# Kernel optimization log

Hardware: AMD Instinct MI355X
Metric: run time of the kernel (lower is better)

## Reference

```python
import jax, jax.numpy as jnp
import numpy as np

B, C, L = 4, 256, 2048
HEADS, DIM_HEAD = 8, 64
HIDDEN = HEADS * DIM_HEAD  # 512


def setup_inputs() -> dict:
    key = jax.random.key(0)
    k1, k2, k3, k4 = jax.random.split(key, 4)
    x = jax.random.normal(k1, (B, C, L), dtype=jnp.float32)
    # Conv1d kernel_size=1 weights, squeezed to [out_ch, in_ch]
    w_qkv = jax.random.normal(k2, (3 * HIDDEN, C), dtype=jnp.float32) * (1.0 / np.sqrt(C))
    w_out = jax.random.normal(k3, (C, HIDDEN), dtype=jnp.float32) * (1.0 / np.sqrt(HIDDEN))
    b_out = jax.random.normal(k4, (C,), dtype=jnp.float32) * 0.01
    return {"x": x, "w_qkv": w_qkv, "w_out": w_out, "b_out": b_out}


def reference(x, w_qkv, w_out, b_out):
    b, c, l = x.shape
    scale = DIM_HEAD ** (-0.5)
    # pointwise conv == channel matmul
    qkv = jnp.einsum('oc,bcl->bol', w_qkv, x)  # [b, 3*hidden, l]
    q, k, v = jnp.split(qkv, 3, axis=1)        # each [b, hidden, l]
    def to_heads(t):
        return t.reshape(b, HEADS, DIM_HEAD, l)  # b h d l
    q, k, v = to_heads(q), to_heads(k), to_heads(v)
    q = q * scale
    sim = jnp.einsum('bhdi,bhdj->bhij', q, k)   # [b,h,l,l]
    attn = jax.nn.softmax(sim, axis=-1)          # stable softmax (max-subtract inside)
    out = jnp.einsum('bhij,bhdj->bhid', attn, v)  # [b,h,l,d]
    out = out.transpose(0, 1, 3, 2).reshape(b, HIDDEN, l)  # b (h d) l
    return jnp.einsum('oc,bcl->bol', w_out, out) + b_out[None, :, None]
```

## Files before the change

### kernel.cpp

```cpp
#include <hip/hip_runtime.h>

typedef unsigned short u16;
typedef unsigned int u32;
typedef __bf16 bf16x8 __attribute__((ext_vector_type(8)));
typedef float f32x4 __attribute__((ext_vector_type(4)));
typedef float f32x16 __attribute__((ext_vector_type(16)));

#define MFMA16(a, b, c) __builtin_amdgcn_mfma_f32_16x16x32_bf16((a), (b), (c), 0, 0, 0)
#define MFMA32(a, b, c) __builtin_amdgcn_mfma_f32_32x32x16_bf16((a), (b), (c), 0, 0, 0)

#define Bn 4
#define Cn 256
#define Ln 2048
#define Hn 8
#define Dn 64
#define HID 512
#define SEGELEMS 4194304

__device__ __forceinline__ u16 bf16_rne(float f) {
  u32 u = __builtin_bit_cast(u32, f);
  u += 0x7FFFu + ((u >> 16) & 1u);
  return (u16)(u >> 16);
}

__device__ __forceinline__ unsigned pack2(float a, float b) {
  return (unsigned)bf16_rne(a) | ((unsigned)bf16_rne(b) << 16);
}

__device__ __forceinline__ u32 pkperm(float lo, float hi) {
  u32 a = __builtin_bit_cast(u32, lo) + 0x8000u;
  u32 b = __builtin_bit_cast(u32, hi) + 0x8000u;
#if __has_builtin(__builtin_amdgcn_perm)
  return __builtin_amdgcn_perm(b, a, 0x07060302u);
#else
  return (b & 0xFFFF0000u) | (a >> 16);
#endif
}

__device__ __forceinline__ float bf16_up(u16 v) {
  u32 u = ((u32)v) << 16;
  return __builtin_bit_cast(float, u);
}

__device__ __forceinline__ float fast_exp2(float x) {
#if __has_builtin(__builtin_amdgcn_exp2f)
  return __builtin_amdgcn_exp2f(x);
#else
  return exp2f(x);
#endif
}

__device__ __forceinline__ float fast_rcp(float x) {
#if __has_builtin(__builtin_amdgcn_rcpf)
  return __builtin_amdgcn_rcpf(x);
#else
  return 1.0f / x;
#endif
}

__device__ __forceinline__ void async_load16(const u16* g, u16* l) {
  __builtin_amdgcn_global_load_lds(
      (const __attribute__((address_space(1))) void*)g,
      (__attribute__((address_space(3))) void*)l, 16, 0, 0);
}

__global__ __launch_bounds__(256) void prep_all(const float* __restrict__ wqkv,
                                                const float* __restrict__ wout,
                                                const float* __restrict__ x,
                                                u16* __restrict__ wq,
                                                u16* __restrict__ wo,
                                                u16* __restrict__ xT) {
  const int t = threadIdx.x;
  if (blockIdx.x < 2048) {
    int i = blockIdx.x * 256 + t;
    const float QSCALE = 0.125f * 1.44269504088896340736f;
    if (i < 3 * HID * Cn) {
      float v = wqkv[i];
      if (i < HID * Cn) v *= QSCALE;
      wq[i] = bf16_rne(v);
    } else {
      int j = i - 3 * HID * Cn;
      wo[j] = bf16_rne(wout[j]);
    }
    return;
  }
  __shared__ u16 tile[64][72];
  int v = blockIdx.x - 2048;
  const int lt = v & 31, ct = (v >> 5) & 3, b = v >> 7;
  const float* xp = x + ((size_t)b * Cn + ct * 64) * Ln + lt * 64;
  for (int pass = 0; pass < 4; ++pass) {
    int c = pass * 16 + (t >> 4);
    int l4 = (t & 15) * 4;
    float4 vf = *(const float4*)(xp + (size_t)c * Ln + l4);
    tile[l4 + 0][c] = bf16_rne(vf.x);
    tile[l4 + 1][c] = bf16_rne(vf.y);
    tile[l4 + 2][c] = bf16_rne(vf.z);
    tile[l4 + 3][c] = bf16_rne(vf.w);
  }
  __syncthreads();
  u16* op = xT + ((size_t)b * Ln + lt * 64) * Cn + ct * 64;
  for (int pass = 0; pass < 2; ++pass) {
    int id = pass * 256 + t;
    int l = id >> 3, c8 = (id & 7) * 8;
    *(uint4*)(op + (size_t)l * Cn + c8) = *(const uint4*)&tile[l][c8];
  }
}

__global__ __launch_bounds__(256, 4) void qkv_gemm(const u16* __restrict__ wq,
                                                   const u16* __restrict__ xT,
                                                   u16* __restrict__ qT,
                                                   u16* __restrict__ kT,
                                                   u16* __restrict__ vv) {
  __shared__ u16 Bs[4096];
  __shared__ u16 Aq[4096];
  __shared__ u16 Ak[4096];
  __shared__ u16 Av[4096];
  const int t = threadIdx.x;
  const int nt = blockIdx.x, head = blockIdx.y, b = blockIdx.z;
  const int n0 = nt * 64, m0 = head * 64;
  const int w = t >> 6, lane = t & 63, q = lane >> 4, ln = lane & 15;

  const u16* Bg = xT + ((size_t)b * Ln + n0) * Cn;
  const u16* AgQ = wq + (size_t)m0 * Cn;
  const u16* AgK = wq + (size_t)(512 + m0) * Cn;
  const u16* AgV = wq + (size_t)(1024 + m0) * Cn;

  f32x4 zf = {0.f, 0.f, 0.f, 0.f};
  f32x4 accQ[4], accK[4], accV[4];
  for (int i = 0; i < 4; ++i) { accQ[i] = zf; accK[i] = zf; accV[i] = zf; }

  const int pr0 = w * 8 + (lane >> 3), pr1 = (4 + w) * 8 + (lane >> 3);
  const int pc0 = (lane & 7) ^ (pr0 & 7), pc1 = (lane & 7) ^ (pr1 & 7);

  for (int kk = 0; kk < 4; ++kk) {
    int k0 = kk * 64;
    async_load16(Bg + (size_t)pr0 * Cn + k0 + pc0 * 8, &Bs[w * 512]);
    async_load16(Bg + (size_t)pr1 * Cn + k0 + pc1 * 8, &Bs[(4 + w) * 512]);
    async_load16(AgQ + (size_t)pr0 * Cn + k0 + pc0 * 8, &Aq[w * 512]);
    async_load16(AgQ + (size_t)pr1 * Cn + k0 + pc1 * 8, &Aq[(4 + w) * 512]);
    async_load16(AgK + (size_t)pr0 * Cn + k0 + pc0 * 8, &Ak[w * 512]);
    async_load16(AgK + (size_t)pr1 * Cn + k0 + pc1 * 8, &Ak[(4 + w) * 512]);
    async_load16(AgV + (size_t)pr0 * Cn + k0 + pc0 * 8, &Av[w * 512]);
    async_load16(AgV + (size_t)pr1 * Cn + k0 + pc1 * 8, &Av[(4 + w) * 512]);
    __syncthreads();
    int ar = w * 16 + ln;
    bf16x8 aq0 = *(const bf16x8*)&Aq[ar * 64 + ((q ^ (ln & 7)) * 8)];
    bf16x8 aq1 = *(const bf16x8*)&Aq[ar * 64 + (((q + 4) ^ (ln & 7)) * 8)];
    bf16x8 ak0 = *(const bf16x8*)&Ak[ar * 64 + ((q ^ (ln & 7)) * 8)];
    bf16x8 ak1 = *(const bf16x8*)&Ak[ar * 64 + (((q + 4) ^ (ln & 7)) * 8)];
    bf16x8 av0 = *(const bf16x8*)&Av[ar * 64 + ((q ^ (ln & 7)) * 8)];
    bf16x8 av1 = *(const bf16x8*)&Av[ar * 64 + (((q + 4) ^ (ln & 7)) * 8)];
    for (int n2 = 0; n2 < 4; ++n2) {
      int br = n2 * 16 + ln;
      bf16x8 b0 = *(const bf16x8*)&Bs[br * 64 + ((q ^ (ln & 7)) * 8)];
      bf16x8 b1 = *(const bf16x8*)&Bs[br * 64 + (((q + 4) ^ (ln & 7)) * 8)];
      accQ[n2] = MFMA16(aq0, b0, accQ[n2]);
      accQ[n2] = MFMA16(aq1, b1, accQ[n2]);
      accK[n2] = MFMA16(ak0, b0, accK[n2]);
      accK[n2] = MFMA16(ak1, b1, accK[n2]);
      accV[n2] = MFMA16(av0, b0, accV[n2]);
      accV[n2] = MFMA16(av1, b1, accV[n2]);
    }
    __syncthreads();
  }

  int od0 = w * 16 + q * 4;
  int cw = od0 >> 3, lo = od0 & 7;
  for (int n2 = 0; n2 < 4; ++n2) {
    int l = n2 * 16 + ln;
    uint2 pk;
    pk.x = pack2(accQ[n2][0], accQ[n2][1]);
    pk.y = pack2(accQ[n2][2], accQ[n2][3]);
    *(uint2*)&Bs[l * 64 + ((cw ^ (l & 7)) * 8) + lo] = pk;
  }
  __syncthreads();
  {
    u16* dst = qT + (((size_t)b * Hn + head) * Ln + n0) * Dn;
    for (int pass = 0; pass < 2; ++pass) {
      int id = pass * 256 + t;
      int l = id >> 3, c = id & 7;
      *(uint4*)(dst + (size_t)l * Dn + c * 8) =
          *(const uint4*)&Bs[l * 64 + ((c ^ (l & 7)) * 8)];
    }
  }
  __syncthreads();
  for (int n2 = 0; n2 < 4; ++n2) {
    int l = n2 * 16 + ln;
    uint2 pk;
    pk.x = pack2(accK[n2][0], accK[n2][1]);
    pk.y = pack2(accK[n2][2], accK[n2][3]);
    *(uint2*)&Bs[l * 64 + ((cw ^ (l & 7)) * 8) + lo] = pk;
  }
  __syncthreads();
  {
    u16* dst = kT + (((size_t)b * Hn + head) * Ln + n0) * Dn;
    for (int pass = 0; pass < 2; ++pass) {
      int id = pass * 256 + t;
      int l = id >> 3, c = id & 7;
      *(uint4*)(dst + (size_t)l * Dn + c * 8) =
          *(const uint4*)&Bs[l * 64 + ((c ^ (l & 7)) * 8)];
    }
  }
  __syncthreads();
  for (int n2 = 0; n2 < 4; ++n2) {
    int l = n2 * 16 + ln;
    int cl = l >> 3, lov = l & 7;
    for (int r = 0; r < 4; ++r) {
      int od = w * 16 + q * 4 + r;
      Bs[od * 64 + ((cl ^ (od & 7)) * 8) + lov] = bf16_rne(accV[n2][r]);
    }
  }
  __syncthreads();
  {
    u16* dst = vv + ((size_t)b * HID + head * 64) * Ln + n0;
    for (int pass = 0; pass < 2; ++pass) {
      int id = pass * 256 + t;
      int od = id >> 3, c = id & 7;
      *(uint4*)(dst + (size_t)od * Ln + c * 8) =
          *(const uint4*)&Bs[od * 64 + ((c ^ (od & 7)) * 8)];
    }
  }
}

__global__ __launch_bounds__(256, 4) void attention(const u16* __restrict__ qT,
                                                    const u16* __restrict__ kT,
                                                    const u16* __restrict__ vv,
                                                    u16* __restrict__ pO,
                                                    float* __restrict__ lP) {
  __shared__ u16 Kt[4096];
  __shared__ u16 Vt[4096];
  __shared__ u16 Ps[8192];
  const int t = threadIdx.x;
  const int qb = blockIdx.x, bh = blockIdx.y, seg = blockIdx.z;
  const int b = bh >> 3, hh = bh & 7;
  const int w = t >> 6, lane = t & 63;
  const int li = lane & 31, h = lane >> 5;
  const int i0 = qb * 128 + w * 32;

  bf16x8 qf0, qf1, qf2, qf3;
  {
    const u16* qrow = qT + (((size_t)bh) * Ln + i0 + li) * Dn + h * 8;
    qf0 = *(const bf16x8*)(qrow + 0);
    qf1 = *(const bf16x8*)(qrow + 16);
    qf2 = *(const bf16x8*)(qrow + 32);
    qf3 = *(const bf16x8*)(qrow + 48);
  }

  const u16* ksrc0 = kT + ((size_t)bh) * Ln * Dn;
  const u16* vsrc0 = vv + ((size_t)b * HID + hh * Dn) * Ln;

  f32x16 z16;
#pragma unroll
  for (int r = 0; r < 16; ++r) z16[r] = 0.f;
  f32x16 o0 = z16, o1 = z16;
  float lp = 0.f;
  u16* pw = Ps + w * 2048;

  const int pr0 = w * 8 + (lane >> 3), pr1 = (4 + w) * 8 + (lane >> 3);
  const int pc0 = (lane & 7) ^ (pr0 & 7), pc1 = (lane & 7) ^ (pr1 & 7);
  const u16* kadr0 = ksrc0 + ((size_t)seg * 1024 + pr0) * Dn + pc0 * 8;
  const u16* kadr1 = ksrc0 + ((size_t)seg * 1024 + pr1) * Dn + pc1 * 8;
  const u16* vadr0 = vsrc0 + (size_t)pr0 * Ln + seg * 1024 + pc0 * 8;
  const u16* vadr1 = vsrc0 + (size_t)pr1 * Ln + seg * 1024 + pc1 * 8;

  const int sw = (li & 7);

  for (int jt = 0; jt < 16; ++jt) {
    int j0 = jt * 64;
    async_load16(kadr0 + (size_t)j0 * Dn, &Kt[w * 512]);
    async_load16(kadr1 + (size_t)j0 * Dn, &Kt[(4 + w) * 512]);
    async_load16(vadr0 + j0, &Vt[w * 512]);
    async_load16(vadr1 + j0, &Vt[(4 + w) * 512]);
    __syncthreads();

    f32x16 sv0, sv1;
    {
      bf16x8 k0 = *(const bf16x8*)&Kt[li * 64 + (((0 + h) ^ sw) * 8)];
      bf16x8 k1 = *(const bf16x8*)&Kt[(32 + li) * 64 + (((0 + h) ^ sw) * 8)];
      sv0 = MFMA32(k0, qf0, z16);
      sv1 = MFMA32(k1, qf0, z16);
    }
    {
      bf16x8 k0 = *(const bf16x8*)&Kt[li * 64 + (((2 + h) ^ sw) * 8)];
      bf16x8 k1 = *(const bf16x8*)&Kt[(32 + li) * 64 + (((2 + h) ^ sw) * 8)];
      sv0 = MFMA32(k0, qf1, sv0);
      sv1 = MFMA32(k1, qf1, sv1);
    }
    {
      bf16x8 k0 = *(const bf16x8*)&Kt[li * 64 + (((4 + h) ^ sw) * 8)];
      bf16x8 k1 = *(const bf16x8*)&Kt[(32 + li) * 64 + (((4 + h) ^ sw) * 8)];
      sv0 = MFMA32(k0, qf2, sv0);
      sv1 = MFMA32(k1, qf2, sv1);
    }
    {
      bf16x8 k0 = *(const bf16x8*)&Kt[li * 64 + (((6 + h) ^ sw) * 8)];
      bf16x8 k1 = *(const bf16x8*)&Kt[(32 + li) * 64 + (((6 + h) ^ sw) * 8)];
      sv0 = MFMA32(k0, qf3, sv0);
      sv1 = MFMA32(k1, qf3, sv1);
    }

#pragma unroll
    for (int js = 0; js < 2; ++js) {
#pragma unroll
      for (int g = 0; g < 4; ++g) {
        float e0 = fast_exp2(js ? sv1[4 * g + 0] : sv0[4 * g + 0]);
        float e1 = fast_exp2(js ? sv1[4 * g + 1] : sv0[4 * g + 1]);
        float e2 = fast_exp2(js ? sv1[4 * g + 2] : sv0[4 * g + 2]);
        float e3 = fast_exp2(js ? sv1[4 * g + 3] : sv0[4 * g + 3]);
        lp += (e0 + e1) + (e2 + e3);
        uint2 pk;
        pk.x = pkperm(e0, e1);
        pk.y = pkperm(e2, e3);
        int cjj = js * 4 + g;
        *(uint2*)&pw[li * 64 + ((cjj ^ sw) * 8) + 4 * h] = pk;
      }
    }

    bf16x8 pf0 = *(const bf16x8*)&pw[li * 64 + (((0 + h) ^ sw) * 8)];
    bf16x8 pf1 = *(const bf16x8*)&pw[li * 64 + (((2 + h) ^ sw) * 8)];
    bf16x8 pf2 = *(const bf16x8*)&pw[li * 64 + (((4 + h) ^ sw) * 8)];
    bf16x8 pf3 = *(const bf16x8*)&pw[li * 64 + (((6 + h) ^ sw) * 8)];
#pragma unroll
    for (int jc = 0; jc < 4; ++jc) {
      int ch = 2 * jc + h;
      bf16x8 pf = (jc == 0) ? pf0 : (jc == 1) ? pf1 : (jc == 2) ? pf2 : pf3;
      bf16x8 vf0 = *(const bf16x8*)&Vt[li * 64 + ((ch ^ sw) * 8)];
      bf16x8 vf1 = *(const bf16x8*)&Vt[(32 + li) * 64 + ((ch ^ sw) * 8)];
      o0 = MFMA32(pf, vf0, o0);
      o1 = MFMA32(pf, vf1, o1);
    }
    __syncthreads();
  }

  float lsum = lp + __shfl_xor(lp, 32);
  if (h == 0)
    lP[(((size_t)seg * Bn + b) * Hn + hh) * Ln + i0 + li] = lsum;
  u16* po = pO + (size_t)seg * SEGELEMS;
#pragma unroll
  for (int r = 0; r < 16; ++r) {
    int ir = (r & 3) + 8 * (r >> 2) + 4 * h;
    size_t base = ((size_t)b * Ln + i0 + ir) * HID + hh * Dn + li;
    po[base] = bf16_rne(o0[r]);
    po[base + 32] = bf16_rne(o1[r]);
  }
}

__global__ __launch_bounds__(256) void combine(const u16* __restrict__ pO,
                                               const float* __restrict__ lP,
                                               u16* __restrict__ attT) {
  int idx8 = (blockIdx.x * 256 + threadIdx.x) * 8;
  int i_lin = idx8 >> 9;
  int h = (idx8 & 511) >> 6;
  int b = i_lin >> 11, i = i_lin & 2047;
  float l = lP[(b * 8 + h) * 2048 + i] + lP[(32 + b * 8 + h) * 2048 + i];
  float s = fast_rcp(l);
  uint4 u0 = *(const uint4*)(pO + idx8);
  uint4 u1 = *(const uint4*)(pO + SEGELEMS + idx8);
  u32 a[4] = {u0.x, u0.y, u0.z, u0.w};
  u32 c[4] = {u1.x, u1.y, u1.z, u1.w};
  uint4 r;
  u32 rw[4];
#pragma unroll
  for (int k = 0; k < 4; ++k) {
    float flo = (bf16_up((u16)(a[k] & 0xFFFF)) + bf16_up((u16)(c[k] & 0xFFFF))) * s;
    float fhi = (bf16_up((u16)(a[k] >> 16)) + bf16_up((u16)(c[k] >> 16))) * s;
    rw[k] = pack2(flo, fhi);
  }
  r.x = rw[0]; r.y = rw[1]; r.z = rw[2]; r.w = rw[3];
  *(uint4*)(attT + idx8) = r;
}

__global__ __launch_bounds__(256, 4) void out_gemm(const u16* __restrict__ wo,
                                                   const u16* __restrict__ attT,
                                                   const float* __restrict__ bout,
                                                   float* __restrict__ out) {
  __shared__ u16 As[4096];
  __shared__ u16 Bs[2048];
  const int t = threadIdx.x;
  const int nt = blockIdx.x, mt = blockIdx.y, b = blockIdx.z;
  const int m0 = mt * 64, n0 = nt * 32;
  const int w = t >> 6, lane = t & 63, q = lane >> 4, ln = lane & 15;

  const u16* Ag = wo + (size_t)m0 * HID;
  const u16* Bg = attT + ((size_t)b * Ln + n0) * HID;

  f32x4 zf = {0.f, 0.f, 0.f, 0.f};
  f32x4 acc[2];
  acc[0] = zf; acc[1] = zf;

  const int pr0 = w * 8 + (lane >> 3), pr1 = (4 + w) * 8 + (lane >> 3);
  const int pc0 = (lane & 7) ^ (pr0 & 7), pc1 = (lane & 7) ^ (pr1 & 7);
  const u16* Aad0 = Ag + (size_t)pr0 * HID + pc0 * 8;
  const u16* Aad1 = Ag + (size_t)pr1 * HID + pc1 * 8;
  const u16* Bad0 = Bg + (size_t)pr0 * HID + pc0 * 8;

#define LOADAB(kk, A0, A1, B0)                   \
  {                                              \
    int k0_ = (kk) * 64;                         \
    A0 = *(const uint4*)(Aad0 + k0_);            \
    A1 = *(const uint4*)(Aad1 + k0_);            \
    B0 = *(const uint4*)(Bad0 + k0_);            \
  }
#define STOREAB(A0, A1, B0)                      \
  {                                              \
    *(uint4*)&As[w * 512 + lane * 8] = A0;       \
    *(uint4*)&As[(4 + w) * 512 + lane * 8] = A1; \
    *(uint4*)&Bs[w * 512 + lane * 8] = B0;       \
  }
#define COMPUTEC()                                                             \
  {                                                                            \
    int ar = w * 16 + ln;                                                      \
    bf16x8 a0 = *(const bf16x8*)&As[ar * 64 + ((q ^ (ln & 7)) * 8)];           \
    bf16x8 a1 = *(const bf16x8*)&As[ar * 64 + (((q + 4) ^ (ln & 7)) * 8)];     \
    for (int n2 = 0; n2 < 2; ++n2) {                                           \
      int br = n2 * 16 + ln;                                                   \
      bf16x8 b0 = *(const bf16x8*)&Bs[br * 64 + ((q ^ (ln & 7)) * 8)];         \
      bf16x8 b1 = *(const bf16x8*)&Bs[br * 64 + (((q + 4) ^ (ln & 7)) * 8)];   \
      acc[n2] = MFMA16(a0, b0, acc[n2]);                                       \
      acc[n2] = MFMA16(a1, b1, acc[n2]);                                       \
    }                                                                          \
  }

  uint4 aa0, aa1, ba0, ab0, ab1, bb0;
  LOADAB(0, aa0, aa1, ba0);
  for (int kk = 0; kk < 8; kk += 2) {
    if (kk) __syncthreads();
    STOREAB(aa0, aa1, ba0);
    __syncthreads();
    LOADAB(kk + 1, ab0, ab1, bb0);
    COMPUTEC();
    __syncthreads();
    STOREAB(ab0, ab1, bb0);
    __syncthreads();
    if (kk + 2 < 8) LOADAB(kk + 2, aa0, aa1, ba0);
    COMPUTEC();
  }
#undef LOADAB
#undef STOREAB
#undef COMPUTEC

  float bias[4];
  for (int r = 0; r < 4; ++r) bias[r] = bout[m0 + w * 16 + q * 4 + r];
  for (int n2 = 0; n2 < 2; ++n2) {
    int l = n0 + n2 * 16 + ln;
    for (int r = 0; r < 4; ++r) {
      int o = m0 + w * 16 + q * 4 + r;
      out[((size_t)b * Cn + o) * Ln + l] = acc[n2][r] + bias[r];
    }
  }
}

extern "C" void kernel_launch(void* const* d_in, const int* in_sizes, int n_in,
                              void* d_out, int out_size, void* d_ws, size_t ws_size,
                              hipStream_t stream) {
  const float* x = (const float*)d_in[0];
  const float* wqkv = (const float*)d_in[1];
  const float* wout = (const float*)d_in[2];
  const float* bout = (const float*)d_in[3];
  float* out = (float*)d_out;
  char* ws = (char*)d_ws;

  u16* wq_b  = (u16*)(ws + 0);
  u16* wo_b  = (u16*)(ws + 786432);
  float* lP  = (float*)(ws + 1048576);
  u16* qT    = (u16*)(ws + 1572864);
  u16* kT    = (u16*)(ws + 9961472);
  u16* vv    = (u16*)(ws + 18350080);
  u16* xT    = (u16*)(ws + 26738688);
  u16* pO    = (u16*)(ws + 26738688);
  u16* attT  = qT;

  prep_all<<<2560, 256, 0, stream>>>(wqkv, wout, x, wq_b, wo_b, xT);
  qkv_gemm<<<dim3(32, 8, 4), 256, 0, stream>>>(wq_b, xT, qT, kT, vv);
  attention<<<dim3(16, 32, 2), 256, 0, stream>>>(qT, kT, vv, pO, lP);
  combine<<<2048, 256, 0, stream>>>(pO, lP, attT);
  out_gemm<<<dim3(64, 4, 4), 256, 0, stream>>>(wo_b, attT, bout, out);
}
```

Baseline: 140.7 us.

## Keep softmax probabilities in registers by permuting V layout to match MFMA output

```diff
diff --git a/kernel.cpp b/kernel.cpp
--- a/kernel.cpp
+++ b/kernel.cpp
@@ -4,6 +4,7 @@
 typedef unsigned int u32;
 typedef __bf16 bf16x8 __attribute__((ext_vector_type(8)));
 typedef float f32x4 __attribute__((ext_vector_type(4)));
+typedef float f32x8 __attribute__((ext_vector_type(8)));
 typedef float f32x16 __attribute__((ext_vector_type(16)));
 
 #define MFMA16(a, b, c) __builtin_amdgcn_mfma_f32_16x16x32_bf16((a), (b), (c), 0, 0, 0)
@@ -25,16 +26,6 @@
 
 __device__ __forceinline__ unsigned pack2(float a, float b) {
   return (unsigned)bf16_rne(a) | ((unsigned)bf16_rne(b) << 16);
-}
-
-__device__ __forceinline__ u32 pkperm(float lo, float hi) {
-  u32 a = __builtin_bit_cast(u32, lo) + 0x8000u;
-  u32 b = __builtin_bit_cast(u32, hi) + 0x8000u;
-#if __has_builtin(__builtin_amdgcn_perm)
-  return __builtin_amdgcn_perm(b, a, 0x07060302u);
-#else
-  return (b & 0xFFFF0000u) | (a >> 16);
-#endif
 }
 
 __device__ __forceinline__ float bf16_up(u16 v) {
@@ -204,7 +195,8 @@
   __syncthreads();
   for (int n2 = 0; n2 < 4; ++n2) {
     int l = n2 * 16 + ln;
-    int cl = l >> 3, lov = l & 7;
+    int lpm = (l & ~12) | ((l & 4) << 1) | ((l & 8) >> 1);
+    int cl = lpm >> 3, lov = lpm & 7;
     for (int r = 0; r < 4; ++r) {
       int od = w * 16 + q * 4 + r;
       Bs[od * 64 + ((cl ^ (od & 7)) * 8) + lov] = bf16_rne(accV[n2][r]);
@@ -229,7 +221,6 @@
                                                     float* __restrict__ lP) {
   __shared__ u16 Kt[4096];
   __shared__ u16 Vt[4096];
-  __shared__ u16 Ps[8192];
   const int t = threadIdx.x;
   const int qb = blockIdx.x, bh = blockIdx.y, seg = blockIdx.z;
   const int b = bh >> 3, hh = bh & 7;
@@ -254,7 +245,6 @@
   for (int r = 0; r < 16; ++r) z16[r] = 0.f;
   f32x16 o0 = z16, o1 = z16;
   float lp = 0.f;
-  u16* pw = Ps + w * 2048;
 
   const int pr0 = w * 8 + (lane >> 3), pr1 = (4 + w) * 8 + (lane >> 3);
   const int pc0 = (lane & 7) ^ (pr0 & 7), pc1 = (lane & 7) ^ (pr1 & 7);
@@ -300,26 +290,20 @@
     }
 
 #pragma unroll
-    for (int js = 0; js < 2; ++js) {
-#pragma unroll
-      for (int g = 0; g < 4; ++g) {
-        float e0 = fast_exp2(js ? sv1[4 * g + 0] : sv0[4 * g + 0]);
-        float e1 = fast_exp2(js ? sv1[4 * g + 1] : sv0[4 * g + 1]);
-        float e2 = fast_exp2(js ? sv1[4 * g + 2] : sv0[4 * g + 2]);
-        float e3 = fast_exp2(js ? sv1[4 * g + 3] : sv0[4 * g + 3]);
-        lp += (e0 + e1) + (e2 + e3);
-        uint2 pk;
-        pk.x = pkperm(e0, e1);
-        pk.y = pkperm(e2, e3);
-        int cjj = js * 4 + g;
-        *(uint2*)&pw[li * 64 + ((cjj ^ sw) * 8) + 4 * h] = pk;
-      }
-    }
-
-    bf16x8 pf0 = *(const bf16x8*)&pw[li * 64 + (((0 + h) ^ sw) * 8)];
-    bf16x8 pf1 = *(const bf16x8*)&pw[li * 64 + (((2 + h) ^ sw) * 8)];
-    bf16x8 pf2 = *(const bf16x8*)&pw[li * 64 + (((4 + h) ^ sw) * 8)];
-    bf16x8 pf3 = *(const bf16x8*)&pw[li * 64 + (((6 + h) ^ sw) * 8)];
+    for (int g = 0; g < 16; ++g) {
+      sv0[g] = fast_exp2(sv0[g]);
+      sv1[g] = fast_exp2(sv1[g]);
+      lp += sv0[g] + sv1[g];
+    }
+    f32x8 e0 = __builtin_shufflevector(sv0, sv0, 0, 1, 2, 3, 4, 5, 6, 7);
+    f32x8 e1 = __builtin_shufflevector(sv0, sv0, 8, 9, 10, 11, 12, 13, 14, 15);
+    f32x8 e2 = __builtin_shufflevector(sv1, sv1, 0, 1, 2, 3, 4, 5, 6, 7);
+    f32x8 e3 = __builtin_shufflevector(sv1, sv1, 8, 9, 10, 11, 12, 13, 14, 15);
+    bf16x8 pf0 = __builtin_convertvector(e0, bf16x8);
+    bf16x8 pf1 = __builtin_convertvector(e1, bf16x8);
+    bf16x8 pf2 = __builtin_convertvector(e2, bf16x8);
+    bf16x8 pf3 = __builtin_convertvector(e3, bf16x8);
+
 #pragma unroll
     for (int jc = 0; jc < 4; ++jc) {
       int ch = 2 * jc + h;
```

After: 136.3 us. -3.1%, faster.
